# Kernel optimization log

Measured on AMD Instinct MI355X. Metric: run time of the kernel, lower is better.

The kernel has to match this reference:

```python
import jax, jax.numpy as jnp
import numpy as np

N = 100000      # nodes
E = 1600000     # edges (avg degree 16)
DIN = 128       # input feature dim
DOUT = 64       # per-head output dim
H = 4           # independent heads, mean-aggregated
LRELU_ALPHA = 0.2  # tf.nn.leaky_relu default


def setup_inputs() -> dict:
    key = jax.random.key(0)
    k = jax.random.split(key, 7)
    inputs = jax.random.normal(k[0], (N, DIN), dtype=jnp.float32)
    edge_row = jnp.sort(jax.random.randint(k[1], (E,), 0, N, dtype=jnp.int32))
    edge_col = jax.random.randint(k[2], (E,), 0, N, dtype=jnp.int32)
    edge_val = jnp.ones((E,), dtype=jnp.float32)  # binary adjacency values
    # Glorot-ish scaled params per head
    W = jax.random.normal(k[3], (H, DIN, DOUT), dtype=jnp.float32) * np.float32(1.0 / np.sqrt(DIN))
    a1 = jax.random.normal(k[4], (H, DOUT), dtype=jnp.float32) * np.float32(1.0 / np.sqrt(DOUT))
    a2 = jax.random.normal(k[5], (H, DOUT), dtype=jnp.float32) * np.float32(1.0 / np.sqrt(DOUT))
    b = jnp.zeros((H, DOUT), dtype=jnp.float32)  # contrib.layers.bias_add bias
    return {"inputs": inputs, "W": W, "a1": a1, "a2": a2, "b": b,
            "edge_val": edge_val, "edge_row": edge_row, "edge_col": edge_col}


def _gat_head(inputs, Wh, a1h, a2h, bh, edge_val, edge_row, edge_col):
    xh = inputs @ Wh                          # [N, DOUT]  per-head projection
    f1 = jax.nn.elu(xh @ a1h)                 # [N]  Dense(D,1, act=elu) on key=x
    f2 = jax.nn.elu(xh @ a2h)                 # [N]
    # sparse_add of adj*f1 (row-broadcast) and adj*f2^T (col-broadcast)
    le = jax.nn.leaky_relu(edge_val * (f1[edge_row] + f2[edge_col]), LRELU_ALPHA)  # [E]
    # sparse softmax per destination row (reverse_axis=1)
    m = jax.ops.segment_max(le, edge_row, num_segments=N)        # [N]
    ex = jnp.exp(le - m[edge_row])                               # [E]
    s = jax.ops.segment_sum(ex, edge_row, num_segments=N)        # [N]
    coef = ex / s[edge_row]                                      # [E]
    # sparse_dense_matmul: out[r] = sum_e coef_e * x[col_e]
    out = jax.ops.segment_sum(coef[:, None] * xh[edge_col], edge_row, num_segments=N)  # [N, DOUT]
    return jax.nn.elu(out + bh)


def reference(inputs, W, a1, a2, b, edge_val, edge_row, edge_col):
    res = jnp.zeros((N, DOUT), dtype=inputs.dtype)
    for h in range(H):  # small fixed head count; each head has independent weights
        res = res + _gat_head(inputs, W[h], a1[h], a2[h], b[h], edge_val, edge_row, edge_col)
    return res / H
```

## Files before the change

### kernel.cpp

```cpp
#include <hip/hip_runtime.h>

#define NN 100000
#define EE 1600000
#define DIN 128
#define DOUT 64
#define NH 4
#define AGG_BLOCKS 2048

typedef __attribute__((ext_vector_type(8))) short bf16x8;
typedef __attribute__((ext_vector_type(4))) float f32x4;

__device__ __forceinline__ float elu_f(float x) {
  return x > 0.f ? x : (__expf(x) - 1.f);
}
__device__ __forceinline__ float b2f(unsigned short u) {
  union { unsigned int i; float f; } v; v.i = ((unsigned int)u) << 16; return v.f;
}
__device__ __forceinline__ unsigned short f2b(float f) {
  union { float f; unsigned int i; } v; v.f = f;
  unsigned int r = v.i + 0x7fffu + ((v.i >> 16) & 1u);
  return (unsigned short)(r >> 16);
}

__global__ __launch_bounds__(256) void prep_k(
    const float* __restrict__ W, unsigned short* __restrict__ wbt,
    const int* __restrict__ erow, int* __restrict__ rp) {
  const int gid = blockIdx.x * 256 + threadIdx.x;
  if (gid < NH * DIN * DOUT) {
    int col = gid >> 7, k = gid & 127;
    int h = col >> 6, j = col & 63;
    wbt[gid] = f2b(W[(size_t)h * DIN * DOUT + k * DOUT + j]);
  }
  if (gid <= NN) {
    int lo = 0, hi = EE;
    while (lo < hi) {
      int mid = (lo + hi) >> 1;
      if (erow[mid] < gid) lo = mid + 1; else hi = mid;
    }
    rp[gid] = lo;
  }
}

__global__ __launch_bounds__(256) void proj_mfma_k(
    const float* __restrict__ inp, const unsigned short* __restrict__ wbt,
    const float* __restrict__ a1, const float* __restrict__ a2,
    float* __restrict__ f1p, float* __restrict__ f2p,
    unsigned short* __restrict__ xh) {
  __shared__ unsigned short lds_a[64 * 128];
  const int tid = threadIdx.x;
  const int h = tid >> 6;
  const int l = tid & 63;
  const int lr = l & 15;
  const int lk = l >> 4;
  const int row0 = blockIdx.x * 64;

  #pragma unroll
  for (int i = 0; i < 8; ++i) {
    const int idx = i * 256 + tid;
    const int row = idx >> 5;
    const int c4 = idx & 31;
    int grow = row0 + row;
    if (grow >= NN) grow = NN - 1;
    const float4 v = *(const float4*)(inp + (size_t)grow * DIN + c4 * 4);
    ushort4 w;
    w.x = f2b(v.x); w.y = f2b(v.y); w.z = f2b(v.z); w.w = f2b(v.w);
    const int byte_off = row * 256 + ((c4 * 8) ^ ((row & 7) << 4));
    *(ushort4*)((char*)lds_a + byte_off) = w;
  }
  __syncthreads();

  f32x4 acc[4][4];
  #pragma unroll
  for (int m = 0; m < 4; ++m)
    #pragma unroll
    for (int n = 0; n < 4; ++n)
      acc[m][n] = (f32x4)(0.f);

  #pragma unroll
  for (int kc = 0; kc < 4; ++kc) {
    bf16x8 bfn[4];
    #pragma unroll
    for (int n = 0; n < 4; ++n)
      bfn[n] = *(const bf16x8*)(wbt + (size_t)(h * DOUT + n * 16 + lr) * DIN +
                                kc * 32 + lk * 8);
    #pragma unroll
    for (int m = 0; m < 4; ++m) {
      const int r = m * 16 + lr;
      const bf16x8 af = *(const bf16x8*)((char*)lds_a + r * 256 +
                                         ((kc * 64 + lk * 16) ^ ((r & 7) << 4)));
      #pragma unroll
      for (int n = 0; n < 4; ++n)
        acc[m][n] = __builtin_amdgcn_mfma_f32_16x16x32_bf16(
            bfn[n], af, acc[m][n], 0, 0, 0);
    }
  }

  float4 a1q[4], a2q[4];
  #pragma unroll
  for (int n = 0; n < 4; ++n) {
    a1q[n] = *(const float4*)(a1 + h * DOUT + n * 16 + lk * 4);
    a2q[n] = *(const float4*)(a2 + h * DOUT + n * 16 + lk * 4);
  }
  #pragma unroll
  for (int m = 0; m < 4; ++m) {
    const int row = row0 + m * 16 + lr;
    const bool ok = row < NN;
    float p1 = 0.f, p2 = 0.f;
    #pragma unroll
    for (int n = 0; n < 4; ++n) {
      const f32x4 a = acc[m][n];
      ushort4 pk;
      pk.x = f2b(a[0]); pk.y = f2b(a[1]); pk.z = f2b(a[2]); pk.w = f2b(a[3]);
      if (ok)
        *(ushort4*)(xh + (size_t)row * (NH * DOUT) + h * DOUT + n * 16 + lk * 4) = pk;
      p1 = fmaf(a[0], a1q[n].x, p1); p1 = fmaf(a[1], a1q[n].y, p1);
      p1 = fmaf(a[2], a1q[n].z, p1); p1 = fmaf(a[3], a1q[n].w, p1);
      p2 = fmaf(a[0], a2q[n].x, p2); p2 = fmaf(a[1], a2q[n].y, p2);
      p2 = fmaf(a[2], a2q[n].z, p2); p2 = fmaf(a[3], a2q[n].w, p2);
    }
    p1 += __shfl_xor(p1, 16); p1 += __shfl_xor(p1, 32);
    p2 += __shfl_xor(p2, 16); p2 += __shfl_xor(p2, 32);
    if (ok && lk == 0) {
      f1p[(size_t)row * NH + h] = elu_f(p1);
      f2p[(size_t)row * NH + h] = elu_f(p2);
    }
  }
}

__global__ __launch_bounds__(256) void agg_k(
    const int* __restrict__ rp, const int* __restrict__ ecol,
    const float* __restrict__ eval, const float* __restrict__ f1p,
    const float* __restrict__ f2p, const unsigned short* __restrict__ xh,
    const float* __restrict__ b, float* __restrict__ out) {
  const int tid = threadIdx.x;
  const int wave = tid >> 6, lane = tid & 63;
  const int wid0 = blockIdx.x * 4 + wave;
  const int g = lane >> 4;
  const float4 bb = *(const float4*)(b + lane * 4);

  for (int r = wid0; r < NN; r += 4 * AGG_BLOCKS) {
    const int e0 = __builtin_amdgcn_readfirstlane(rp[r]);
    const int e1 = __builtin_amdgcn_readfirstlane(rp[r + 1]);
    const float f1r = f1p[(size_t)r * NH + g];
    float ax = 0.f, ay = 0.f, az = 0.f, aw = 0.f;
    float ssum = 0.f;
    int e = e0;
    for (; e + 8 <= e1; e += 8) {
      int c[8]; float vv[8];
      #pragma unroll
      for (int u = 0; u < 8; ++u) { c[u] = ecol[e + u]; vv[u] = eval[e + u]; }
      ushort4 xv[8]; float f2v[8];
      #pragma unroll
      for (int u = 0; u < 8; ++u) {
        xv[u] = *(const ushort4*)(xh + (size_t)c[u] * (NH * DOUT) + lane * 4);
        f2v[u] = f2p[(size_t)c[u] * NH + g];
      }
      #pragma unroll
      for (int u = 0; u < 8; ++u) {
        const float t = vv[u] * (f1r + f2v[u]);
        const float ex = __expf(fmaxf(t, 0.2f * t));
        ssum += ex;
        ax = fmaf(ex, b2f(xv[u].x), ax);
        ay = fmaf(ex, b2f(xv[u].y), ay);
        az = fmaf(ex, b2f(xv[u].z), az);
        aw = fmaf(ex, b2f(xv[u].w), aw);
      }
    }
    if (e < e1) {
      int c[8]; float vv[8]; bool okk[8];
      #pragma unroll
      for (int u = 0; u < 8; ++u) {
        int ee = e + u;
        okk[u] = ee < e1;
        if (!okk[u]) ee = e1 - 1;
        c[u] = ecol[ee]; vv[u] = eval[ee];
      }
      ushort4 xv[8]; float f2v[8];
      #pragma unroll
      for (int u = 0; u < 8; ++u) {
        xv[u] = *(const ushort4*)(xh + (size_t)c[u] * (NH * DOUT) + lane * 4);
        f2v[u] = f2p[(size_t)c[u] * NH + g];
      }
      #pragma unroll
      for (int u = 0; u < 8; ++u) {
        const float t = vv[u] * (f1r + f2v[u]);
        float ex = __expf(fmaxf(t, 0.2f * t));
        ex = okk[u] ? ex : 0.f;
        ssum += ex;
        ax = fmaf(ex, b2f(xv[u].x), ax);
        ay = fmaf(ex, b2f(xv[u].y), ay);
        az = fmaf(ex, b2f(xv[u].z), az);
        aw = fmaf(ex, b2f(xv[u].w), aw);
      }
    }
    const float inv = (e1 > e0) ? (1.f / ssum) : 0.f;
    float v0 = elu_f(ax * inv + bb.x);
    float v1 = elu_f(ay * inv + bb.y);
    float v2 = elu_f(az * inv + bb.z);
    float v3 = elu_f(aw * inv + bb.w);
    v0 += __shfl_xor(v0, 16); v1 += __shfl_xor(v1, 16);
    v2 += __shfl_xor(v2, 16); v3 += __shfl_xor(v3, 16);
    v0 += __shfl_xor(v0, 32); v1 += __shfl_xor(v1, 32);
    v2 += __shfl_xor(v2, 32); v3 += __shfl_xor(v3, 32);
    if (lane < 16) {
      f32x4 o = {v0 * 0.25f, v1 * 0.25f, v2 * 0.25f, v3 * 0.25f};
      __builtin_nontemporal_store(o, (f32x4*)(out + (size_t)r * DOUT + lane * 4));
    }
  }
}

extern "C" void kernel_launch(void* const* d_in, const int* in_sizes, int n_in,
                              void* d_out, int out_size, void* d_ws, size_t ws_size,
                              hipStream_t stream) {
  const float* inp = (const float*)d_in[0];
  const float* W   = (const float*)d_in[1];
  const float* a1  = (const float*)d_in[2];
  const float* a2  = (const float*)d_in[3];
  const float* b   = (const float*)d_in[4];
  const float* ev  = (const float*)d_in[5];
  const int* erow  = (const int*)d_in[6];
  const int* ecol  = (const int*)d_in[7];
  float* out = (float*)d_out;

  char* ws = (char*)d_ws;
  size_t off = 0;
  int* rp = (int*)(ws + off);
  off += (((size_t)(NN + 1) * 4) + 255) & ~(size_t)255;
  float* f1p = (float*)(ws + off);
  off += (((size_t)NH * NN * 4) + 255) & ~(size_t)255;
  float* f2p = (float*)(ws + off);
  off += (((size_t)NH * NN * 4) + 255) & ~(size_t)255;
  unsigned short* xh = (unsigned short*)(ws + off);
  off += (((size_t)NN * NH * DOUT * 2) + 255) & ~(size_t)255;
  unsigned short* wbt = (unsigned short*)(ws + off);

  prep_k<<<(NN + 1 + 255) / 256, 256, 0, stream>>>(W, wbt, erow, rp);
  proj_mfma_k<<<(NN + 63) / 64, 256, 0, stream>>>(inp, wbt, a1, a2, f1p, f2p, xh);
  agg_k<<<AGG_BLOCKS, 256, 0, stream>>>(rp, ecol, ev, f1p, f2p, xh, b, out);
}
```

Before: 189.3 us.

## Stage projection output through LDS for coalesced stores; one row per wave aggregation

The projection kernel now writes its bf16 results into shared memory, in two halves split by head pair, and then emits fully coalesced 16-byte row-contiguous stores to xh. Before, each lane wrote scattered 8-byte pieces. The aggregation kernel drops its grid-stride loop and launches one wave per destination row, and it loads edge indices with nontemporal hints. The cost is extra barriers and LDS traffic in the projection kernel, plus many more small blocks in the aggregation launch.

Result: faster. 172.1 us, median of 2 (-9.1%).

```diff
diff --git a/kernel.cpp b/kernel.cpp
--- a/kernel.cpp
+++ b/kernel.cpp
@@ -5,7 +5,6 @@
 #define DIN 128
 #define DOUT 64
 #define NH 4
-#define AGG_BLOCKS 2048
 
 typedef __attribute__((ext_vector_type(8))) short bf16x8;
 typedef __attribute__((ext_vector_type(4))) float f32x4;
@@ -101,18 +100,13 @@
     a1q[n] = *(const float4*)(a1 + h * DOUT + n * 16 + lk * 4);
     a2q[n] = *(const float4*)(a2 + h * DOUT + n * 16 + lk * 4);
   }
+  float p1m[4], p2m[4];
   #pragma unroll
   for (int m = 0; m < 4; ++m) {
-    const int row = row0 + m * 16 + lr;
-    const bool ok = row < NN;
     float p1 = 0.f, p2 = 0.f;
     #pragma unroll
     for (int n = 0; n < 4; ++n) {
       const f32x4 a = acc[m][n];
-      ushort4 pk;
-      pk.x = f2b(a[0]); pk.y = f2b(a[1]); pk.z = f2b(a[2]); pk.w = f2b(a[3]);
-      if (ok)
-        *(ushort4*)(xh + (size_t)row * (NH * DOUT) + h * DOUT + n * 16 + lk * 4) = pk;
       p1 = fmaf(a[0], a1q[n].x, p1); p1 = fmaf(a[1], a1q[n].y, p1);
       p1 = fmaf(a[2], a1q[n].z, p1); p1 = fmaf(a[3], a1q[n].w, p1);
       p2 = fmaf(a[0], a2q[n].x, p2); p2 = fmaf(a[1], a2q[n].y, p2);
@@ -120,9 +114,45 @@
     }
     p1 += __shfl_xor(p1, 16); p1 += __shfl_xor(p1, 32);
     p2 += __shfl_xor(p2, 16); p2 += __shfl_xor(p2, 32);
-    if (ok && lk == 0) {
-      f1p[(size_t)row * NH + h] = elu_f(p1);
-      f2p[(size_t)row * NH + h] = elu_f(p2);
+    p1m[m] = p1; p2m[m] = p2;
+  }
+
+  #pragma unroll
+  for (int half = 0; half < 2; ++half) {
+    __syncthreads();
+    if ((h >> 1) == half) {
+      #pragma unroll
+      for (int m = 0; m < 4; ++m) {
+        const int row = m * 16 + lr;
+        #pragma unroll
+        for (int n = 0; n < 4; ++n) {
+          const f32x4 a = acc[m][n];
+          ushort4 pk;
+          pk.x = f2b(a[0]); pk.y = f2b(a[1]); pk.z = f2b(a[2]); pk.w = f2b(a[3]);
+          const int colb = (h & 1) * 128 + n * 32 + lk * 8;
+          *(ushort4*)((char*)lds_a + row * 256 + (colb ^ ((row & 7) << 4))) = pk;
+        }
+      }
+    }
+    __syncthreads();
+    #pragma unroll
+    for (int i = 0; i < 4; ++i) {
+      const int idx = i * 256 + tid;
+      const int row = idx >> 4, c = idx & 15;
+      const f32x4 v = *(const f32x4*)((char*)lds_a + row * 256 +
+                                      ((c * 16) ^ ((row & 7) << 4)));
+      const int grow = row0 + row;
+      if (grow < NN)
+        *(f32x4*)((char*)xh + (size_t)grow * 512 + half * 256 + c * 16) = v;
+    }
+  }
+
+  #pragma unroll
+  for (int m = 0; m < 4; ++m) {
+    const int row = row0 + m * 16 + lr;
+    if (row < NN && lk == 0) {
+      f1p[(size_t)row * NH + h] = elu_f(p1m[m]);
+      f2p[(size_t)row * NH + h] = elu_f(p2m[m]);
     }
   }
 }
@@ -134,78 +164,79 @@
     const float* __restrict__ b, float* __restrict__ out) {
   const int tid = threadIdx.x;
   const int wave = tid >> 6, lane = tid & 63;
-  const int wid0 = blockIdx.x * 4 + wave;
+  const int r = blockIdx.x * 4 + wave;
+  if (r >= NN) return;
   const int g = lane >> 4;
+  const int e0 = __builtin_amdgcn_readfirstlane(rp[r]);
+  const int e1 = __builtin_amdgcn_readfirstlane(rp[r + 1]);
+  const float f1r = f1p[(size_t)r * NH + g];
+  float ax = 0.f, ay = 0.f, az = 0.f, aw = 0.f;
+  float ssum = 0.f;
+  int e = e0;
+  for (; e + 8 <= e1; e += 8) {
+    int c[8]; float vv[8];
+    #pragma unroll
+    for (int u = 0; u < 8; ++u) {
+      c[u] = __builtin_nontemporal_load(ecol + e + u);
+      vv[u] = __builtin_nontemporal_load(eval + e + u);
+    }
+    ushort4 xv[8]; float f2v[8];
+    #pragma unroll
+    for (int u = 0; u < 8; ++u) {
+      xv[u] = *(const ushort4*)(xh + (size_t)c[u] * (NH * DOUT) + lane * 4);
+      f2v[u] = f2p[(size_t)c[u] * NH + g];
+    }
+    #pragma unroll
+    for (int u = 0; u < 8; ++u) {
+      const float t = vv[u] * (f1r + f2v[u]);
+      const float ex = __expf(fmaxf(t, 0.2f * t));
+      ssum += ex;
+      ax = fmaf(ex, b2f(xv[u].x), ax);
+      ay = fmaf(ex, b2f(xv[u].y), ay);
+      az = fmaf(ex, b2f(xv[u].z), az);
+      aw = fmaf(ex, b2f(xv[u].w), aw);
+    }
+  }
+  if (e < e1) {
+    int c[8]; float vv[8]; bool okk[8];
+    #pragma unroll
+    for (int u = 0; u < 8; ++u) {
+      int ee = e + u;
+      okk[u] = ee < e1;
+      if (!okk[u]) ee = e1 - 1;
+      c[u] = ecol[ee]; vv[u] = eval[ee];
+    }
+    ushort4 xv[8]; float f2v[8];
+    #pragma unroll
+    for (int u = 0; u < 8; ++u) {
+      xv[u] = *(const ushort4*)(xh + (size_t)c[u] * (NH * DOUT) + lane * 4);
+      f2v[u] = f2p[(size_t)c[u] * NH + g];
+    }
+    #pragma unroll
+    for (int u = 0; u < 8; ++u) {
+      const float t = vv[u] * (f1r + f2v[u]);
+      float ex = __expf(fmaxf(t, 0.2f * t));
+      ex = okk[u] ? ex : 0.f;
+      ssum += ex;
+      ax = fmaf(ex, b2f(xv[u].x), ax);
+      ay = fmaf(ex, b2f(xv[u].y), ay);
+      az = fmaf(ex, b2f(xv[u].z), az);
+      aw = fmaf(ex, b2f(xv[u].w), aw);
+    }
+  }
   const float4 bb = *(const float4*)(b + lane * 4);
-
-  for (int r = wid0; r < NN; r += 4 * AGG_BLOCKS) {
-    const int e0 = __builtin_amdgcn_readfirstlane(rp[r]);
-    const int e1 = __builtin_amdgcn_readfirstlane(rp[r + 1]);
-    const float f1r = f1p[(size_t)r * NH + g];
-    float ax = 0.f, ay = 0.f, az = 0.f, aw = 0.f;
-    float ssum = 0.f;
-    int e = e0;
-    for (; e + 8 <= e1; e += 8) {
-      int c[8]; float vv[8];
-      #pragma unroll
-      for (int u = 0; u < 8; ++u) { c[u] = ecol[e + u]; vv[u] = eval[e + u]; }
-      ushort4 xv[8]; float f2v[8];
-      #pragma unroll
-      for (int u = 0; u < 8; ++u) {
-        xv[u] = *(const ushort4*)(xh + (size_t)c[u] * (NH * DOUT) + lane * 4);
-        f2v[u] = f2p[(size_t)c[u] * NH + g];
-      }
-      #pragma unroll
-      for (int u = 0; u < 8; ++u) {
-        const float t = vv[u] * (f1r + f2v[u]);
-        const float ex = __expf(fmaxf(t, 0.2f * t));
-        ssum += ex;
-        ax = fmaf(ex, b2f(xv[u].x), ax);
-        ay = fmaf(ex, b2f(xv[u].y), ay);
-        az = fmaf(ex, b2f(xv[u].z), az);
-        aw = fmaf(ex, b2f(xv[u].w), aw);
-      }
-    }
-    if (e < e1) {
-      int c[8]; float vv[8]; bool okk[8];
-      #pragma unroll
-      for (int u = 0; u < 8; ++u) {
-        int ee = e + u;
-        okk[u] = ee < e1;
-        if (!okk[u]) ee = e1 - 1;
-        c[u] = ecol[ee]; vv[u] = eval[ee];
-      }
-      ushort4 xv[8]; float f2v[8];
-      #pragma unroll
-      for (int u = 0; u < 8; ++u) {
-        xv[u] = *(const ushort4*)(xh + (size_t)c[u] * (NH * DOUT) + lane * 4);
-        f2v[u] = f2p[(size_t)c[u] * NH + g];
-      }
-      #pragma unroll
-      for (int u = 0; u < 8; ++u) {
-        const float t = vv[u] * (f1r + f2v[u]);
-        float ex = __expf(fmaxf(t, 0.2f * t));
-        ex = okk[u] ? ex : 0.f;
-        ssum += ex;
-        ax = fmaf(ex, b2f(xv[u].x), ax);
-        ay = fmaf(ex, b2f(xv[u].y), ay);
-        az = fmaf(ex, b2f(xv[u].z), az);
-        aw = fmaf(ex, b2f(xv[u].w), aw);
-      }
-    }
-    const float inv = (e1 > e0) ? (1.f / ssum) : 0.f;
-    float v0 = elu_f(ax * inv + bb.x);
-    float v1 = elu_f(ay * inv + bb.y);
-    float v2 = elu_f(az * inv + bb.z);
-    float v3 = elu_f(aw * inv + bb.w);
-    v0 += __shfl_xor(v0, 16); v1 += __shfl_xor(v1, 16);
-    v2 += __shfl_xor(v2, 16); v3 += __shfl_xor(v3, 16);
-    v0 += __shfl_xor(v0, 32); v1 += __shfl_xor(v1, 32);
-    v2 += __shfl_xor(v2, 32); v3 += __shfl_xor(v3, 32);
-    if (lane < 16) {
-      f32x4 o = {v0 * 0.25f, v1 * 0.25f, v2 * 0.25f, v3 * 0.25f};
-      __builtin_nontemporal_store(o, (f32x4*)(out + (size_t)r * DOUT + lane * 4));
-    }
+  const float inv = (e1 > e0) ? (1.f / ssum) : 0.f;
+  float v0 = elu_f(ax * inv + bb.x);
+  float v1 = elu_f(ay * inv + bb.y);
+  float v2 = elu_f(az * inv + bb.z);
+  float v3 = elu_f(aw * inv + bb.w);
+  v0 += __shfl_xor(v0, 16); v1 += __shfl_xor(v1, 16);
+  v2 += __shfl_xor(v2, 16); v3 += __shfl_xor(v3, 16);
+  v0 += __shfl_xor(v0, 32); v1 += __shfl_xor(v1, 32);
+  v2 += __shfl_xor(v2, 32); v3 += __shfl_xor(v3, 32);
+  if (lane < 16) {
+    f32x4 o = {v0 * 0.25f, v1 * 0.25f, v2 * 0.25f, v3 * 0.25f};
+    __builtin_nontemporal_store(o, (f32x4*)(out + (size_t)r * DOUT + lane * 4));
   }
 }
 
@@ -236,5 +267,5 @@
 
   prep_k<<<(NN + 1 + 255) / 256, 256, 0, stream>>>(W, wbt, erow, rp);
   proj_mfma_k<<<(NN + 63) / 64, 256, 0, stream>>>(inp, wbt, a1, a2, f1p, f2p, xh);
-  agg_k<<<AGG_BLOCKS, 256, 0, stream>>>(rp, ecol, ev, f1p, f2p, xh, b, out);
-}
+  agg_k<<<(NN + 3) / 4, 256, 0, stream>>>(rp, ecol, ev, f1p, f2p, xh, b, out);
+}
```
